# Performance work log

Hardware: AMD Instinct MI355X
Metric: run time of the kernel (lower is better)

The kernel has to match this reference:

```python
import jax, jax.numpy as jnp
import numpy as np

# dims
B, HID = 16, 2048            # batch (decode tokens), hidden size
NH, NKV, HD = 16, 8, 128     # q heads, kv heads, head dim (GQA group = 2)
BLK, MAXB = 16, 256          # block size, max blocks per sequence
NBLOCKS = B * MAXB           # total cache blocks (disjoint per sequence)
MAXPOS = 8192
EPS = 1e-6
THETA = 1000000.0
SCALE = HD ** -0.5
Q_SIZE, KV_SIZE = NH * HD, NKV * HD


def _rms(x, w):
    # RMSNorm over last dim (per-head), like NormLayer._normalize
    return x * jax.lax.rsqrt(jnp.mean(x * x, axis=-1, keepdims=True) + EPS) * w


def _rotate(x, cos, sin):
    x1, x2 = jnp.split(x, 2, axis=-1)
    return jnp.concatenate([x1 * cos - x2 * sin, x2 * cos + x1 * sin], axis=-1)


def setup_inputs() -> dict:
    key = jax.random.key(0)
    ks = jax.random.split(key, 8)
    hidden_states = jax.random.normal(ks[0], (B, HID), jnp.float32)
    qkv_w = jax.random.normal(ks[1], (Q_SIZE + 2 * KV_SIZE, HID), jnp.float32) * 0.02
    o_w = jax.random.normal(ks[2], (HID, Q_SIZE), jnp.float32) * 0.02
    q_norm_w = jnp.ones((HD,), jnp.float32)
    k_norm_w = jnp.ones((HD,), jnp.float32)
    k_cache = jax.random.normal(ks[3], (NBLOCKS, BLK, NKV, HD), jnp.float32) * 0.5
    v_cache = jax.random.normal(ks[4], (NBLOCKS, BLK, NKV, HD), jnp.float32) * 0.5
    # disjoint block tables per sequence
    block_tables = jnp.arange(B * MAXB, dtype=jnp.int32).reshape(B, MAXB)
    # context length includes the newly written token (vLLM decode convention)
    context_lens = jax.random.randint(ks[5], (B,), 1, MAXB * BLK + 1).astype(jnp.int32)
    positions = context_lens - 1  # position of the current decode token
    slot_mapping = (block_tables[jnp.arange(B), positions // BLK] * BLK + positions % BLK).astype(jnp.int32)
    # RoPE cache: [max_pos, 1, HD] = cat(cos, sin) over half-dim
    inv_freq = 1.0 / (THETA ** (jnp.arange(0, HD, 2, dtype=jnp.float32) / HD))
    freqs = jnp.arange(MAXPOS, dtype=jnp.float32)[:, None] * inv_freq[None, :]
    cos_sin_cache = jnp.concatenate([jnp.cos(freqs), jnp.sin(freqs)], axis=-1)[:, None, :]
    return dict(hidden_states=hidden_states, positions=positions, qkv_w=qkv_w,
                q_norm_w=q_norm_w, k_norm_w=k_norm_w, o_w=o_w,
                cos_sin_cache=cos_sin_cache, k_cache=k_cache, v_cache=v_cache,
                slot_mapping=slot_mapping, block_tables=block_tables,
                context_lens=context_lens)


def reference(hidden_states, positions, qkv_w, q_norm_w, k_norm_w, o_w,
              cos_sin_cache, k_cache, v_cache, slot_mapping, block_tables,
              context_lens):
    # fused QKV projection (no bias -> QK-norm path)
    qkv = hidden_states @ qkv_w.T
    q, k, v = jnp.split(qkv, [Q_SIZE, Q_SIZE + KV_SIZE], axis=-1)
    q = _rms(q.reshape(B, NH, HD), q_norm_w)
    k = _rms(k.reshape(B, NKV, HD), k_norm_w)
    v = v.reshape(B, NKV, HD)
    # RoPE
    cs = cos_sin_cache[positions]            # [B, 1, HD]
    cos, sin = jnp.split(cs, 2, axis=-1)     # [B, 1, HD/2] each
    q = _rotate(q, cos, sin)
    k = _rotate(k, cos, sin)
    # write new k/v into paged cache at slot_mapping
    D = NKV * HD
    kc = k_cache.reshape(-1, D).at[slot_mapping].set(k.reshape(B, D)).reshape(k_cache.shape)
    vc = v_cache.reshape(-1, D).at[slot_mapping].set(v.reshape(B, D)).reshape(v_cache.shape)
    # paged decode attention: gather blocks, mask by context length
    L = MAXB * BLK
    K = kc[block_tables].reshape(B, L, NKV, HD)
    V = vc[block_tables].reshape(B, L, NKV, HD)
    qg = q.reshape(B, NKV, NH // NKV, HD)    # GQA grouping
    scores = jnp.einsum('bkgd,blkd->bkgl', qg, K) * SCALE
    valid = (jnp.arange(L)[None, :] < context_lens[:, None])[:, None, None, :]
    scores = jnp.where(valid, scores, -jnp.inf)
    p = jax.nn.softmax(scores, axis=-1)
    out = jnp.einsum('bkgl,blkd->bkgd', p, V).reshape(B, Q_SIZE)
    return out @ o_w.T
```

## Files before the change

kernel.cpp:

```cpp
#include <hip/hip_runtime.h>
#include <hip/hip_bf16.h>
#include <cstddef>

#define BATCH    16
#define HID      2048
#define NH       16
#define NKV      8
#define HD       128
#define BLKSZ    16
#define MAXB     256
#define LMAX     4096
#define QSIZE    2048
#define KVSIZE   1024
#define QKVROWS  4096
#define KDIM     2048
#define EPS      1e-6f
#define SCALE    0.08838834764831845f

#define CHUNK    64
#define NCHUNK   64
#define PSTRIDE  130

__global__ __launch_bounds__(256) void gemm_m16(const float* __restrict__ x,
                                                const float* __restrict__ w,
                                                float* __restrict__ out,
                                                int ostride) {
    __shared__ float wt[16][132];
    __shared__ float ht[16][132];
    const int t  = threadIdx.x;
    const int r  = t >> 4;
    const int b  = t & 15;
    const int lr = t >> 4;
    const int c8 = (t & 15) * 8;
    const int row0 = blockIdx.x * 16;

    const float* wl = w + (size_t)(row0 + lr) * KDIM + c8;
    const float* xl = x + (size_t)lr * KDIM + c8;

    float acc = 0.f;
    for (int kc = 0; kc < KDIM; kc += 128) {
        float4 a0 = *(const float4*)(wl + kc);
        float4 a1 = *(const float4*)(wl + kc + 4);
        float4 b0 = *(const float4*)(xl + kc);
        float4 b1 = *(const float4*)(xl + kc + 4);
        __syncthreads();
        *(float4*)&wt[lr][c8]     = a0;
        *(float4*)&wt[lr][c8 + 4] = a1;
        *(float4*)&ht[lr][c8]     = b0;
        *(float4*)&ht[lr][c8 + 4] = b1;
        __syncthreads();
#pragma unroll
        for (int k = 0; k < 128; k += 4) {
            float4 wv = *(const float4*)&wt[r][k];
            float4 hv = *(const float4*)&ht[b][k];
            acc += wv.x * hv.x + wv.y * hv.y + wv.z * hv.z + wv.w * hv.w;
        }
    }
    out[(size_t)b * ostride + row0 + r] = acc;
}

__global__ __launch_bounds__(64) void norm_rope_cache(float* __restrict__ qkv,
                                                      const float* __restrict__ qw,
                                                      const float* __restrict__ kw,
                                                      const float* __restrict__ cs_cache,
                                                      const int* __restrict__ positions,
                                                      const int* __restrict__ slot_mapping,
                                                      float* __restrict__ k_cache,
                                                      float* __restrict__ v_cache) {
    const int s = blockIdx.x;
    const int b = blockIdx.y;
    const int l = threadIdx.x;
    float* base = qkv + (size_t)b * QKVROWS;

    if (s < NH) {
        float* src = base + s * HD;
        float x1 = src[l], x2 = src[l + 64];
        float ss = x1 * x1 + x2 * x2;
#pragma unroll
        for (int m = 1; m < 64; m <<= 1) ss += __shfl_xor(ss, m, 64);
        float inv = rsqrtf(ss * (1.f / 128.f) + EPS);
        x1 = x1 * inv * qw[l];
        x2 = x2 * inv * qw[l + 64];
        int pos = positions[b];
        float c  = cs_cache[(size_t)pos * HD + l];
        float sn = cs_cache[(size_t)pos * HD + 64 + l];
        src[l]      = (x1 * c - x2 * sn) * SCALE;
        src[l + 64] = (x2 * c + x1 * sn) * SCALE;
    } else if (s < NH + NKV) {
        int h = s - NH;
        const float* src = base + QSIZE + h * HD;
        float x1 = src[l], x2 = src[l + 64];
        float ss = x1 * x1 + x2 * x2;
#pragma unroll
        for (int m = 1; m < 64; m <<= 1) ss += __shfl_xor(ss, m, 64);
        float inv = rsqrtf(ss * (1.f / 128.f) + EPS);
        x1 = x1 * inv * kw[l];
        x2 = x2 * inv * kw[l + 64];
        int pos = positions[b];
        float c  = cs_cache[(size_t)pos * HD + l];
        float sn = cs_cache[(size_t)pos * HD + 64 + l];
        int slot = slot_mapping[b];
        float* dst = k_cache + (size_t)slot * KVSIZE + h * HD;
        dst[l]      = x1 * c - x2 * sn;
        dst[l + 64] = x2 * c + x1 * sn;
    } else {
        int h = s - NH - NKV;
        const float* src = base + QSIZE + KVSIZE + h * HD;
        int slot = slot_mapping[b];
        float* dst = v_cache + (size_t)slot * KVSIZE + h * HD;
        dst[l]      = src[l];
        dst[l + 64] = src[l + 64];
    }
}

__global__ __launch_bounds__(256) void attn_partial(const float* __restrict__ q,
                                                    const float* __restrict__ k_cache,
                                                    const float* __restrict__ v_cache,
                                                    const int* __restrict__ block_tables,
                                                    const int* __restrict__ context_lens,
                                                    float* __restrict__ part) {
    const int b    = blockIdx.z;
    const int kv   = blockIdx.y;
    const int wave = threadIdx.x >> 6;
    const int chunk = blockIdx.x * 4 + wave;
    const int lane = threadIdx.x & 63;
    const int len  = context_lens[b];
    const int start = chunk * CHUNK;
    if (start >= len) return;

    const int t = lane >> 2;
    const int c = lane & 3;

    const float* qb = q + (size_t)b * QKVROWS + (2 * kv) * HD + c * 32;
    float q0[32], q1[32];
#pragma unroll
    for (int j = 0; j < 32; j += 4) {
        *(float4*)&q0[j] = *(const float4*)(qb + j);
        *(float4*)&q1[j] = *(const float4*)(qb + HD + j);
    }

    float acc0[32], acc1[32];
#pragma unroll
    for (int j = 0; j < 32; j++) { acc0[j] = 0.f; acc1[j] = 0.f; }
    float m0 = -1e30f, m1 = -1e30f, l0 = 0.f, l1 = 0.f;

    const int* btab = block_tables + b * MAXB;
    const int nblk = min(CHUNK / BLKSZ, (len - start + BLKSZ - 1) >> 4);

    for (int cb = 0; cb < nblk; cb++) {
        const int gb = (start >> 4) + cb;
        const int pb = btab[gb];
        const float* kp = k_cache + ((size_t)pb * BLKSZ + t) * KVSIZE + kv * HD + c * 32;
        const float* vp = v_cache + ((size_t)pb * BLKSZ + t) * KVSIZE + kv * HD + c * 32;
        float4 kx[8], vx[8];
#pragma unroll
        for (int j = 0; j < 8; j++) kx[j] = ((const float4*)kp)[j];
#pragma unroll
        for (int j = 0; j < 8; j++) vx[j] = ((const float4*)vp)[j];

        float s0 = 0.f, s1 = 0.f;
#pragma unroll
        for (int j = 0; j < 8; j++) {
            const float* kk = (const float*)&kx[j];
#pragma unroll
            for (int e = 0; e < 4; e++) {
                s0 += q0[4 * j + e] * kk[e];
                s1 += q1[4 * j + e] * kk[e];
            }
        }
        s0 += __shfl_xor(s0, 1, 64); s0 += __shfl_xor(s0, 2, 64);
        s1 += __shfl_xor(s1, 1, 64); s1 += __shfl_xor(s1, 2, 64);

        const int gidx = start + cb * BLKSZ + t;
        if (gidx >= len) { s0 = -1e30f; s1 = -1e30f; }

        float bm0 = s0, bm1 = s1;
#pragma unroll
        for (int m = 4; m < 64; m <<= 1) {
            bm0 = fmaxf(bm0, __shfl_xor(bm0, m, 64));
            bm1 = fmaxf(bm1, __shfl_xor(bm1, m, 64));
        }
        const float nm0 = fmaxf(m0, bm0), nm1 = fmaxf(m1, bm1);
        const float a0 = __expf(m0 - nm0), a1 = __expf(m1 - nm1);
        const float p0 = __expf(s0 - nm0), p1 = __expf(s1 - nm1);
        m0 = nm0; m1 = nm1;
        l0 = l0 * a0 + p0;
        l1 = l1 * a1 + p1;
#pragma unroll
        for (int j = 0; j < 8; j++) {
            const float* vv = (const float*)&vx[j];
#pragma unroll
            for (int e = 0; e < 4; e++) {
                acc0[4 * j + e] = acc0[4 * j + e] * a0 + p0 * vv[e];
                acc1[4 * j + e] = acc1[4 * j + e] * a1 + p1 * vv[e];
            }
        }
    }

#pragma unroll
    for (int m = 4; m < 64; m <<= 1) {
#pragma unroll
        for (int j = 0; j < 32; j++) {
            acc0[j] += __shfl_xor(acc0[j], m, 64);
            acc1[j] += __shfl_xor(acc1[j], m, 64);
        }
    }
#pragma unroll
    for (int m = 1; m < 64; m <<= 1) {
        l0 += __shfl_xor(l0, m, 64);
        l1 += __shfl_xor(l1, m, 64);
    }
    l0 *= 0.25f; l1 *= 0.25f;

    float* pp0 = part + (size_t)(((b * NKV + kv) * NCHUNK + chunk) * 2 + 0) * PSTRIDE;
    float* pp1 = pp0 + PSTRIDE;
    if (t == 0) {
#pragma unroll
        for (int j = 0; j < 32; j++) {
            pp0[2 + c * 32 + j] = acc0[j];
            pp1[2 + c * 32 + j] = acc1[j];
        }
        if (c == 0) {
            pp0[0] = m0; pp0[1] = l0;
            pp1[0] = m1; pp1[1] = l1;
        }
    }
}

__global__ __launch_bounds__(128) void attn_reduce(const float* __restrict__ part,
                                                   const int* __restrict__ context_lens,
                                                   float* __restrict__ attn_out) {
    const int h = blockIdx.x;
    const int b = blockIdx.y;
    const int d = threadIdx.x;
    const int kv = h >> 1, g = h & 1;
    const int len = context_lens[b];
    const int nch = (len + CHUNK - 1) / CHUNK;

    const float* pb = part + (size_t)(((b * NKV + kv) * NCHUNK) * 2 + g) * PSTRIDE;
    float M = -1e30f;
    for (int i = 0; i < nch; i++) M = fmaxf(M, pb[(size_t)i * 2 * PSTRIDE]);
    float L = 0.f, acc = 0.f;
    for (int i = 0; i < nch; i++) {
        const float* e = pb + (size_t)i * 2 * PSTRIDE;
        float wgt = __expf(e[0] - M);
        L   += wgt * e[1];
        acc += wgt * e[2 + d];
    }
    attn_out[(size_t)b * QSIZE + h * HD + d] = acc / L;
}

extern "C" void kernel_launch(void* const* d_in, const int* in_sizes, int n_in,
                              void* d_out, int out_size, void* d_ws, size_t ws_size,
                              hipStream_t stream) {
    const float* hidden        = (const float*)d_in[0];
    const int*   positions     = (const int*)d_in[1];
    const float* qkv_w         = (const float*)d_in[2];
    const float* q_norm_w      = (const float*)d_in[3];
    const float* k_norm_w      = (const float*)d_in[4];
    const float* o_w           = (const float*)d_in[5];
    const float* cs_cache      = (const float*)d_in[6];
    float*       k_cache       = (float*)d_in[7];
    float*       v_cache       = (float*)d_in[8];
    const int*   slot_mapping  = (const int*)d_in[9];
    const int*   block_tables  = (const int*)d_in[10];
    const int*   context_lens  = (const int*)d_in[11];
    float*       out           = (float*)d_out;

    char* ws = (char*)d_ws;
    float* qkv      = (float*)(ws);
    float* attn_out = (float*)(ws + (size_t)BATCH * QKVROWS * 4);
    float* part     = (float*)(ws + (size_t)BATCH * QKVROWS * 4
                                  + (size_t)BATCH * QSIZE * 4);

    gemm_m16<<<dim3(QKVROWS / 16), 256, 0, stream>>>(hidden, qkv_w, qkv, QKVROWS);
    norm_rope_cache<<<dim3(NH + 2 * NKV, BATCH), 64, 0, stream>>>(
        qkv, q_norm_w, k_norm_w, cs_cache, positions, slot_mapping, k_cache, v_cache);
    attn_partial<<<dim3(NCHUNK / 4, NKV, BATCH), 256, 0, stream>>>(
        qkv, k_cache, v_cache, block_tables, context_lens, part);
    attn_reduce<<<dim3(NH, BATCH), 128, 0, stream>>>(part, context_lens, attn_out);
    gemm_m16<<<dim3(HID / 16), 256, 0, stream>>>(attn_out, o_w, out, HID);
}
```

Baseline: 619.1 us.

## Rewrite skinny GEMM as register-tiled split-K with LDS reduction; prefetch block table

Replaces the LDS-staged 16x16 tile GEMM with a kernel where each wave streams two weight rows across the full K in float4 loads and multiplies them against all 16 batch rows held in registers. Partial sums are reduced through shared memory. This removes the two syncthreads per K step and increases memory-level parallelism on the weight stream, which dominates the decode GEMMs. The attention kernel also preloads its four block-table entries up front, so the dependent loads are no longer serialized inside the loop. The cost is higher register pressure (32 accumulators plus 16 float4 activations per thread) and redundant activation reads across waves.

```diff
diff --git a/kernel.cpp b/kernel.cpp
--- a/kernel.cpp
+++ b/kernel.cpp
@@ -21,42 +21,62 @@
 #define NCHUNK   64
 #define PSTRIDE  130
 
-__global__ __launch_bounds__(256) void gemm_m16(const float* __restrict__ x,
-                                                const float* __restrict__ w,
-                                                float* __restrict__ out,
-                                                int ostride) {
-    __shared__ float wt[16][132];
-    __shared__ float ht[16][132];
-    const int t  = threadIdx.x;
-    const int r  = t >> 4;
-    const int b  = t & 15;
-    const int lr = t >> 4;
-    const int c8 = (t & 15) * 8;
-    const int row0 = blockIdx.x * 16;
-
-    const float* wl = w + (size_t)(row0 + lr) * KDIM + c8;
-    const float* xl = x + (size_t)lr * KDIM + c8;
-
-    float acc = 0.f;
-    for (int kc = 0; kc < KDIM; kc += 128) {
-        float4 a0 = *(const float4*)(wl + kc);
-        float4 a1 = *(const float4*)(wl + kc + 4);
-        float4 b0 = *(const float4*)(xl + kc);
-        float4 b1 = *(const float4*)(xl + kc + 4);
-        __syncthreads();
-        *(float4*)&wt[lr][c8]     = a0;
-        *(float4*)&wt[lr][c8 + 4] = a1;
-        *(float4*)&ht[lr][c8]     = b0;
-        *(float4*)&ht[lr][c8 + 4] = b1;
-        __syncthreads();
-#pragma unroll
-        for (int k = 0; k < 128; k += 4) {
-            float4 wv = *(const float4*)&wt[r][k];
-            float4 hv = *(const float4*)&ht[b][k];
-            acc += wv.x * hv.x + wv.y * hv.y + wv.z * hv.z + wv.w * hv.w;
-        }
-    }
-    out[(size_t)b * ostride + row0 + r] = acc;
+#define GROWS    8
+
+__global__ __launch_bounds__(256) void gemm_m16_v3(const float* __restrict__ x,
+                                                   const float* __restrict__ w,
+                                                   float* __restrict__ out,
+                                                   int ostride) {
+    __shared__ float red[4][32][68];
+    const int t    = threadIdx.x;
+    const int wv   = t >> 6;
+    const int lane = t & 63;
+    const int row0 = blockIdx.x * GROWS + wv * 2;
+
+    const float* w0 = w + (size_t)row0 * KDIM + lane * 4;
+    const float* w1 = w0 + KDIM;
+    const float* xb = x + lane * 4;
+
+    float acc[2][16];
+#pragma unroll
+    for (int r = 0; r < 2; r++)
+#pragma unroll
+        for (int b = 0; b < 16; b++) acc[r][b] = 0.f;
+
+#pragma unroll 2
+    for (int it = 0; it < 8; it++) {
+        const int ko = it * 256;
+        float4 wr0 = *(const float4*)(w0 + ko);
+        float4 wr1 = *(const float4*)(w1 + ko);
+        float4 xv[16];
+#pragma unroll
+        for (int b = 0; b < 16; b++)
+            xv[b] = *(const float4*)(xb + (size_t)b * KDIM + ko);
+#pragma unroll
+        for (int b = 0; b < 16; b++) {
+            acc[0][b] += wr0.x * xv[b].x + wr0.y * xv[b].y + wr0.z * xv[b].z + wr0.w * xv[b].w;
+            acc[1][b] += wr1.x * xv[b].x + wr1.y * xv[b].y + wr1.z * xv[b].z + wr1.w * xv[b].w;
+        }
+    }
+
+#pragma unroll
+    for (int r = 0; r < 2; r++)
+#pragma unroll
+        for (int b = 0; b < 16; b++)
+            red[wv][r * 16 + b][lane] = acc[r][b];
+    __syncthreads();
+
+    if (t < 128) {
+        const int R = t >> 4, b = t & 15;
+        const float* src = &red[R >> 1][(R & 1) * 16 + b][0];
+        float s = 0.f;
+#pragma unroll
+        for (int i = 0; i < 16; i++) {
+            float4 v = *(const float4*)(src + i * 4);
+            s += v.x + v.y + v.z + v.w;
+        }
+        out[(size_t)b * ostride + blockIdx.x * GROWS + R] = s;
+    }
 }
 
 __global__ __launch_bounds__(64) void norm_rope_cache(float* __restrict__ qkv,
@@ -131,6 +151,11 @@
     const int t = lane >> 2;
     const int c = lane & 3;
 
+    const int* btab = block_tables + b * MAXB;
+    int pbuf[4];
+#pragma unroll
+    for (int i = 0; i < 4; i++) pbuf[i] = btab[(start >> 4) + i];
+
     const float* qb = q + (size_t)b * QKVROWS + (2 * kv) * HD + c * 32;
     float q0[32], q1[32];
 #pragma unroll
@@ -144,12 +169,10 @@
     for (int j = 0; j < 32; j++) { acc0[j] = 0.f; acc1[j] = 0.f; }
     float m0 = -1e30f, m1 = -1e30f, l0 = 0.f, l1 = 0.f;
 
-    const int* btab = block_tables + b * MAXB;
     const int nblk = min(CHUNK / BLKSZ, (len - start + BLKSZ - 1) >> 4);
 
     for (int cb = 0; cb < nblk; cb++) {
-        const int gb = (start >> 4) + cb;
-        const int pb = btab[gb];
+        const int pb = pbuf[cb];
         const float* kp = k_cache + ((size_t)pb * BLKSZ + t) * KVSIZE + kv * HD + c * 32;
         const float* vp = v_cache + ((size_t)pb * BLKSZ + t) * KVSIZE + kv * HD + c * 32;
         float4 kx[8], vx[8];
@@ -273,11 +296,11 @@
     float* part     = (float*)(ws + (size_t)BATCH * QKVROWS * 4
                                   + (size_t)BATCH * QSIZE * 4);
 
-    gemm_m16<<<dim3(QKVROWS / 16), 256, 0, stream>>>(hidden, qkv_w, qkv, QKVROWS);
+    gemm_m16_v3<<<dim3(QKVROWS / GROWS), 256, 0, stream>>>(hidden, qkv_w, qkv, QKVROWS);
     norm_rope_cache<<<dim3(NH + 2 * NKV, BATCH), 64, 0, stream>>>(
         qkv, q_norm_w, k_norm_w, cs_cache, positions, slot_mapping, k_cache, v_cache);
     attn_partial<<<dim3(NCHUNK / 4, NKV, BATCH), 256, 0, stream>>>(
         qkv, k_cache, v_cache, block_tables, context_lens, part);
     attn_reduce<<<dim3(NH, BATCH), 128, 0, stream>>>(part, context_lens, attn_out);
-    gemm_m16<<<dim3(HID / 16), 256, 0, stream>>>(attn_out, o_w, out, HID);
-}
+    gemm_m16_v3<<<dim3(HID / GROWS), 256, 0, stream>>>(attn_out, o_w, out, HID);
+}
```

Result: no change. 620.9 us (+0.3%).
